# Kernel optimization log

Measured on AMD Instinct MI355X. Metric: run time of the kernel, lower is better.

The kernel has to match this reference:

```python
import jax, jax.numpy as jnp
import numpy as np

N = 50000
IN_DIM, HID_DIM, OUT_DIM = 16, 64, 32


def setup_inputs() -> dict:
    key = jax.random.key(0)
    k1, k2, k3, k4, k5 = jax.random.split(key, 5)
    x = jax.random.normal(k1, (N, IN_DIM), dtype=jnp.float32)
    edge_index = jax.random.randint(k2, (2, 800000), 0, N, dtype=jnp.int64)
    # GCNConv weights (glorot-ish scale) and biases
    W1 = jax.random.normal(k3, (IN_DIM, HID_DIM), dtype=jnp.float32) / np.sqrt(IN_DIM)
    b1 = jnp.zeros((HID_DIM,), dtype=jnp.float32)
    W2 = jax.random.normal(k4, (HID_DIM, OUT_DIM), dtype=jnp.float32) / np.sqrt(HID_DIM)
    b2 = jnpplus = jnp.zeros((OUT_DIM,), dtype=jnp.float32)
    return {"x": x, "edge_index": edge_index, "W1": W1, "b1": b1, "W2": W2, "b2": b2}


def _gcn_conv(x, src, dst, norm, W, b, num_nodes):
    # PyG GCNConv: h = X W; out[d] = sum_e norm_e * h[src_e]; out += b
    h = x @ W                                   # [N, D_out] small GEMM
    msgs = h[src] * norm[:, None]               # [E+N, D_out] gather (memory-bound)
    out = jax.ops.segment_sum(msgs, dst, num_segments=num_nodes)  # scatter-add
    return out + b


def reference(x, edge_index, W1, b1, W2, b2):
    num_nodes = x.shape[0]
    # add self-loops (PyG GCNConv default add_self_loops=True)
    loops = jnp.arange(num_nodes, dtype=edge_index.dtype)
    src = jnp.concatenate([edge_index[0], loops])
    dst = jnp.concatenate([edge_index[1], loops])
    # symmetric normalization D^{-1/2} (A+I) D^{-1/2}, degree over dst
    deg = jax.ops.segment_sum(jnp.ones_like(src, dtype=x.dtype), dst, num_segments=num_nodes)
    dinv = jnp.where(deg > 0, jax.lax.rsqrt(deg), 0.0)
    norm = dinv[src] * dinv[dst]                # [E+N]

    h = _gcn_conv(x, src, dst, norm, W1, b1, num_nodes)
    h = jax.nn.relu(h)
    out = _gcn_conv(h, src, dst, norm, W2, b2, num_nodes)
    return out
```

## Files before the change

kernel.cpp:

```cpp
#include <hip/hip_runtime.h>
#include <hip/hip_fp16.h>

#define IN_DIM  16
#define HID_DIM 64
#define OUT_DIM 32

#define CAP   8192
#define EPB   3328
#define CONVB 64

__device__ __forceinline__ int detect_is64(const void* edges) {
    const int* w = (const int*)edges;
    int is64 = 1;
    #pragma unroll
    for (int i = 0; i < 16; ++i) is64 &= (w[2 * i + 1] == 0);
    return is64;
}

__device__ __forceinline__ long long edge_at(const void* edges, int is64, long long i) {
    if (is64) return ((const long long*)edges)[i];
    return (long long)((const int*)edges)[i];
}

__global__ __launch_bounds__(256) void k_partA(const void* edges, int* gcur,
                                               unsigned int* gpart, int nbuk, long long E,
                                               const float* __restrict__ x,
                                               __half* __restrict__ xh,
                                               long long xElems, int nblkA) {
    if (blockIdx.x >= nblkA) {
        const float4* x4 = (const float4*)x;
        uint2* outp = (uint2*)xh;
        long long n4 = xElems >> 2;
        for (long long i = (long long)(blockIdx.x - nblkA) * 256 + threadIdx.x;
             i < n4; i += (long long)CONVB * 256) {
            float4 v = x4[i];
            __half2 a = __floats2half2_rn(v.x, v.y);
            __half2 b = __floats2half2_rn(v.z, v.w);
            outp[i] = make_uint2(*(unsigned int*)&a, *(unsigned int*)&b);
        }
        return;
    }

    __shared__ unsigned int staged[EPB];
    __shared__ int hcnt[256], hoff[256], hcur[256];
    __shared__ int s64s;
    int t = threadIdx.x;
    if (t == 0) s64s = detect_is64(edges);
    hcnt[t] = 0;
    __syncthreads();
    int is64 = s64s;

    long long e0 = (long long)blockIdx.x * EPB;
    unsigned int rs[13], rd[13];
    int nval = 0;
    #pragma unroll
    for (int k = 0; k < 13; ++k) {
        long long e = e0 + t + k * 256;
        if (e < E) {
            rs[k] = (unsigned int)edge_at(edges, is64, e);
            rd[k] = (unsigned int)edge_at(edges, is64, E + e);
            atomicAdd(&hcnt[rd[k] >> 8], 1);
            nval = k + 1;
        }
    }
    __syncthreads();

    int v = hcnt[t];
    hoff[t] = v;
    __syncthreads();
    for (int d = 1; d < 256; d <<= 1) {
        int u = (t >= d) ? hoff[t - d] : 0;
        __syncthreads();
        hoff[t] += u;
        __syncthreads();
    }
    int excl = hoff[t] - v;
    hoff[t] = excl;
    hcur[t] = excl;
    __syncthreads();

    #pragma unroll
    for (int k = 0; k < 13; ++k) {
        if (k < nval) {
            int p = atomicAdd(&hcur[rd[k] >> 8], 1);
            staged[p] = rs[k] | ((rd[k] & 255u) << 16);
        }
    }
    __syncthreads();

    if (t < nbuk) {
        int c = hcnt[t];
        if (c > 0) {
            int base = atomicAdd(&gcur[t], c);
            int o = hoff[t];
            for (int k = 0; k < c; ++k) {
                int idx = base + k;
                if (idx < CAP) gpart[(size_t)t * CAP + idx] = staged[o + k];
            }
        }
    }
}

__global__ __launch_bounds__(256) void k_partB(const int* __restrict__ gcur,
                                               const unsigned int* __restrict__ gpart,
                                               unsigned short* __restrict__ csr,
                                               int* __restrict__ offs,
                                               float* __restrict__ dinv,
                                               int nbuk, int N) {
    __shared__ unsigned int ebuf[CAP];
    __shared__ int bscan[256];
    __shared__ int hcnt[256], hoff[256], hcur[256];
    int t = threadIdx.x;
    int b = blockIdx.x;

    int bc = (t < nbuk) ? min(gcur[t], CAP) : 0;
    bscan[t] = bc;
    hcnt[t] = 0;
    __syncthreads();
    for (int d = 1; d < 256; d <<= 1) {
        int u = (t >= d) ? bscan[t - d] : 0;
        __syncthreads();
        bscan[t] += u;
        __syncthreads();
    }
    int base = (b == 0) ? 0 : bscan[b - 1];
    int cnt  = bscan[b] - base;

    for (int i = t; i < cnt; i += 256) ebuf[i] = gpart[(size_t)b * CAP + i];
    __syncthreads();
    for (int i = t; i < cnt; i += 256) atomicAdd(&hcnt[(ebuf[i] >> 16) & 255u], 1);
    __syncthreads();

    int v = hcnt[t];
    hoff[t] = v;
    __syncthreads();
    for (int d = 1; d < 256; d <<= 1) {
        int u = (t >= d) ? hoff[t - d] : 0;
        __syncthreads();
        hoff[t] += u;
        __syncthreads();
    }
    int excl = hoff[t] - v;
    hcur[t] = excl;
    __syncthreads();

    int node = b * 256 + t;
    if (node < N) {
        offs[node] = base + excl;
        dinv[node] = rsqrtf((float)v + 1.0f);
    }
    if (b == nbuk - 1 && t == 0) offs[N] = bscan[nbuk - 1];

    for (int i = t; i < cnt; i += 256) {
        unsigned int e = ebuf[i];
        int dl = (e >> 16) & 255;
        int p = atomicAdd(&hcur[dl], 1);
        csr[base + p] = (unsigned short)(e & 0xffffu);
    }
}

#define ASTR 17
#define H1S  68
__global__ __launch_bounds__(256) void k_agg1g(
    const __half* __restrict__ xh, const float* __restrict__ dinv,
    const int* __restrict__ offs, const unsigned short* __restrict__ csr,
    const float* __restrict__ W1, const float* __restrict__ b1,
    const float* __restrict__ W2, __half* __restrict__ h2, int N)
{
    __shared__ __align__(16) float W1s[IN_DIM * HID_DIM];
    __shared__ __align__(16) float W2s[HID_DIM * OUT_DIM];
    __shared__ float b1s[HID_DIM];
    __shared__ __align__(16) float aggs[16 * ASTR];
    __shared__ __align__(16) float h1s[16 * H1S];

    int tid = threadIdx.x;
    for (int i = tid; i < IN_DIM * HID_DIM; i += 256) W1s[i] = W1[i];
    for (int i = tid; i < HID_DIM * OUT_DIM; i += 256) W2s[i] = W2[i];
    if (tid < HID_DIM) b1s[tid] = b1[tid];

    int lane = tid & 63;
    int g = lane >> 4, sub = lane & 15;
    int comp = sub >> 3;
    int way  = sub & 7;
    int nl   = (tid >> 6) * 4 + g;
    int node = blockIdx.x * 16 + nl;

    float acc[8] = {0.f, 0.f, 0.f, 0.f, 0.f, 0.f, 0.f, 0.f};
    float di = 0.f;
    if (node < N) {
        const uint4* x2 = (const uint4*)xh;
        di = dinv[node];
        int start = offs[node], end = offs[node + 1];
        if (way == 0) {
            uint4 r = x2[(size_t)node * 2 + comp];
            const __half2* hp = (const __half2*)&r;
            #pragma unroll
            for (int c = 0; c < 4; ++c) {
                float2 f = __half22float2(hp[c]);
                acc[c * 2]     = di * f.x;
                acc[c * 2 + 1] = di * f.y;
            }
        }
        int j = start + way;
        for (; j + 8 < end; j += 16) {
            int s0 = csr[j], s1 = csr[j + 8];
            float w0 = dinv[s0], w1 = dinv[s1];
            uint4 r0 = x2[(size_t)s0 * 2 + comp];
            uint4 r1 = x2[(size_t)s1 * 2 + comp];
            const __half2* hp0 = (const __half2*)&r0;
            const __half2* hp1 = (const __half2*)&r1;
            #pragma unroll
            for (int c = 0; c < 4; ++c) {
                float2 f0 = __half22float2(hp0[c]);
                float2 f1 = __half22float2(hp1[c]);
                acc[c * 2]     += w0 * f0.x + w1 * f1.x;
                acc[c * 2 + 1] += w0 * f0.y + w1 * f1.y;
            }
        }
        if (j < end) {
            int s = csr[j];
            float w = dinv[s];
            uint4 r = x2[(size_t)s * 2 + comp];
            const __half2* hp = (const __half2*)&r;
            #pragma unroll
            for (int c = 0; c < 4; ++c) {
                float2 f = __half22float2(hp[c]);
                acc[c * 2]     += w * f.x;
                acc[c * 2 + 1] += w * f.y;
            }
        }
        #pragma unroll
        for (int m = 1; m <= 4; m <<= 1) {
            #pragma unroll
            for (int c = 0; c < 8; ++c) acc[c] += __shfl_xor(acc[c], m, 64);
        }
    }
    if (way == 0) {
        #pragma unroll
        for (int c = 0; c < 8; ++c) aggs[nl * ASTR + comp * 8 + c] = di * acc[c];
    }
    __syncthreads();

    int nl2 = tid >> 4, q = tid & 15;

    float a1[4];
    #pragma unroll
    for (int c = 0; c < 4; ++c) a1[c] = b1s[q * 4 + c];
    #pragma unroll
    for (int k = 0; k < IN_DIM; ++k) {
        float a = aggs[nl2 * ASTR + k];
        float4 w = *(const float4*)&W1s[k * HID_DIM + q * 4];
        a1[0] += a * w.x; a1[1] += a * w.y; a1[2] += a * w.z; a1[3] += a * w.w;
    }
    *(float4*)&h1s[nl2 * H1S + q * 4] =
        make_float4(fmaxf(a1[0], 0.f), fmaxf(a1[1], 0.f),
                    fmaxf(a1[2], 0.f), fmaxf(a1[3], 0.f));
    __syncthreads();

    float a2x = 0.f, a2y = 0.f;
    const float4* h1row = (const float4*)&h1s[nl2 * H1S];
    #pragma unroll
    for (int k4 = 0; k4 < 16; ++k4) {
        float4 hv = h1row[k4];
        const float* wb = &W2s[(k4 * 4) * OUT_DIM + q * 2];
        float2 w0 = *(const float2*)(wb);
        float2 w1 = *(const float2*)(wb + OUT_DIM);
        float2 w2 = *(const float2*)(wb + 2 * OUT_DIM);
        float2 w3 = *(const float2*)(wb + 3 * OUT_DIM);
        a2x += hv.x * w0.x + hv.y * w1.x + hv.z * w2.x + hv.w * w3.x;
        a2y += hv.x * w0.y + hv.y * w1.y + hv.z * w2.y + hv.w * w3.y;
    }
    int gn = blockIdx.x * 16 + nl2;
    if (gn < N) {
        __half2 p = __floats2half2_rn(a2x, a2y);
        ((unsigned int*)h2)[(size_t)gn * 16 + q] = *(unsigned int*)&p;
    }
}

__global__ __launch_bounds__(256) void k_agg2(
    const __half* __restrict__ h2, const float* __restrict__ dinv,
    const int* __restrict__ offs, const unsigned short* __restrict__ csr,
    const float* __restrict__ b2, float* __restrict__ out, int N)
{
    int gtid = blockIdx.x * 256 + threadIdx.x;
    int lane = gtid & 63;
    int g = lane >> 4, sub = lane & 15;
    int comp = sub & 3, way = sub >> 2;
    int node = (gtid >> 6) * 4 + g;
    if (node >= N) return;
    const uint4* h24 = (const uint4*)h2;
    float di = dinv[node];
    int start = offs[node], end = offs[node + 1];
    float acc[8] = {0.f, 0.f, 0.f, 0.f, 0.f, 0.f, 0.f, 0.f};
    if (way == 0) {
        uint4 r = h24[(size_t)node * 4 + comp];
        const __half2* hp = (const __half2*)&r;
        #pragma unroll
        for (int c = 0; c < 4; ++c) {
            float2 f = __half22float2(hp[c]);
            acc[c * 2]     = di * f.x;
            acc[c * 2 + 1] = di * f.y;
        }
    }
    int j = start + way;
    for (; j + 4 < end; j += 8) {
        int s0 = csr[j], s1 = csr[j + 4];
        float w0 = dinv[s0], w1 = dinv[s1];
        uint4 r0 = h24[(size_t)s0 * 4 + comp];
        uint4 r1 = h24[(size_t)s1 * 4 + comp];
        const __half2* hp0 = (const __half2*)&r0;
        const __half2* hp1 = (const __half2*)&r1;
        #pragma unroll
        for (int c = 0; c < 4; ++c) {
            float2 f0 = __half22float2(hp0[c]);
            float2 f1 = __half22float2(hp1[c]);
            acc[c * 2]     += w0 * f0.x + w1 * f1.x;
            acc[c * 2 + 1] += w0 * f0.y + w1 * f1.y;
        }
    }
    if (j < end) {
        int s = csr[j];
        float w = dinv[s];
        uint4 r = h24[(size_t)s * 4 + comp];
        const __half2* hp = (const __half2*)&r;
        #pragma unroll
        for (int c = 0; c < 4; ++c) {
            float2 f = __half22float2(hp[c]);
            acc[c * 2]     += w * f.x;
            acc[c * 2 + 1] += w * f.y;
        }
    }
    #pragma unroll
    for (int m = 4; m <= 8; m <<= 1) {
        #pragma unroll
        for (int c = 0; c < 8; ++c) acc[c] += __shfl_xor(acc[c], m, 64);
    }
    if (way == 0) {
        const float4* b24 = (const float4*)b2;
        float4 bb0 = b24[comp * 2], bb1 = b24[comp * 2 + 1];
        float4* out4 = (float4*)out;
        out4[(size_t)node * 8 + comp * 2 + 0] =
            make_float4(di * acc[0] + bb0.x, di * acc[1] + bb0.y,
                        di * acc[2] + bb0.z, di * acc[3] + bb0.w);
        out4[(size_t)node * 8 + comp * 2 + 1] =
            make_float4(di * acc[4] + bb1.x, di * acc[5] + bb1.y,
                        di * acc[6] + bb1.z, di * acc[7] + bb1.w);
    }
}

extern "C" void kernel_launch(void* const* d_in, const int* in_sizes, int n_in,
                              void* d_out, int out_size, void* d_ws, size_t ws_size,
                              hipStream_t stream) {
    const float* x     = (const float*)d_in[0];
    const void*  edges = d_in[1];
    const float* W1    = (const float*)d_in[2];
    const float* b1    = (const float*)d_in[3];
    const float* W2    = (const float*)d_in[4];
    const float* b2    = (const float*)d_in[5];
    float* out = (float*)d_out;

    const int       N = in_sizes[0] / IN_DIM;
    const long long E = in_sizes[1] / 2;
    const int    NBUK = (N + 255) >> 8;
    const int   NBLKA = (int)((E + EPB - 1) / EPB);

    unsigned short* csr   = (unsigned short*)d_ws;
    unsigned int*   gpart = (unsigned int*)(csr + ((E + 7) & ~7LL));
    __half* xh       = (__half*)(gpart + (size_t)NBUK * CAP);
    __half* h2       = (__half*)(xh + (size_t)IN_DIM * N);
    float*  dinv     = (float*)(h2 + (size_t)OUT_DIM * N);
    int*    offs     = (int*)(dinv + N);
    int*    gcur     = offs + N + 1;

    const int B = 256;
    hipMemsetAsync(gcur, 0, (size_t)NBUK * sizeof(int), stream);
    k_partA<<<NBLKA + CONVB, B, 0, stream>>>(edges, gcur, gpart, NBUK, E,
                                             x, xh, (long long)N * IN_DIM, NBLKA);
    k_partB<<<NBUK, B, 0, stream>>>(gcur, gpart, csr, offs, dinv, NBUK, N);

    k_agg1g<<<(N + 15) / 16, B, 0, stream>>>(xh, dinv, offs, csr,
                                             W1, b1, W2, h2, N);
    k_agg2<<<(N + 15) / 16, B, 0, stream>>>(h2, dinv, offs, csr, b2, out, N);
}
```

Baseline: 137.2 us.

## Use wavefront shuffle scans, hoist CSR loads, add occupancy launch bounds

Replaces the shared-memory Hillis-Steele scans (sixteen block barriers each) in the partition kernels with a wave-level shuffle scan followed by a short cross-wave combine. It also moves the dinv/offs loads in k_agg1g ahead of the weight staging so their latency overlaps it. It adds min-blocks-per-CU hints to the two aggregation kernels to raise occupancy. The hints may force register spills.

```diff
diff --git a/kernel.cpp b/kernel.cpp
--- a/kernel.cpp
+++ b/kernel.cpp
@@ -20,6 +20,23 @@
 __device__ __forceinline__ long long edge_at(const void* edges, int is64, long long i) {
     if (is64) return ((const long long*)edges)[i];
     return (long long)((const int*)edges)[i];
+}
+
+__device__ __forceinline__ int block_incl_scan(int v, int t, int* wsum) {
+    int lane = t & 63, w = t >> 6;
+    int s = v;
+    #pragma unroll
+    for (int d = 1; d < 64; d <<= 1) {
+        int u = __shfl_up(s, d, 64);
+        if (lane >= d) s += u;
+    }
+    if (lane == 63) wsum[w] = s;
+    __syncthreads();
+    int add = 0;
+    #pragma unroll
+    for (int i = 0; i < 4; ++i)
+        if (i < w) add += wsum[i];
+    return s + add;
 }
 
 __global__ __launch_bounds__(256) void k_partA(const void* edges, int* gcur,
@@ -43,6 +60,7 @@
 
     __shared__ unsigned int staged[EPB];
     __shared__ int hcnt[256], hoff[256], hcur[256];
+    __shared__ int wsum[4];
     __shared__ int s64s;
     int t = threadIdx.x;
     if (t == 0) s64s = detect_is64(edges);
@@ -66,15 +84,8 @@
     __syncthreads();
 
     int v = hcnt[t];
-    hoff[t] = v;
-    __syncthreads();
-    for (int d = 1; d < 256; d <<= 1) {
-        int u = (t >= d) ? hoff[t - d] : 0;
-        __syncthreads();
-        hoff[t] += u;
-        __syncthreads();
-    }
-    int excl = hoff[t] - v;
+    int incl = block_incl_scan(v, t, wsum);
+    int excl = incl - v;
     hoff[t] = excl;
     hcur[t] = excl;
     __syncthreads();
@@ -109,20 +120,16 @@
                                                int nbuk, int N) {
     __shared__ unsigned int ebuf[CAP];
     __shared__ int bscan[256];
-    __shared__ int hcnt[256], hoff[256], hcur[256];
+    __shared__ int hcnt[256], hcur[256];
+    __shared__ int wsum[4];
     int t = threadIdx.x;
     int b = blockIdx.x;
 
     int bc = (t < nbuk) ? min(gcur[t], CAP) : 0;
-    bscan[t] = bc;
     hcnt[t] = 0;
-    __syncthreads();
-    for (int d = 1; d < 256; d <<= 1) {
-        int u = (t >= d) ? bscan[t - d] : 0;
-        __syncthreads();
-        bscan[t] += u;
-        __syncthreads();
-    }
+    int bincl = block_incl_scan(bc, t, wsum);
+    bscan[t] = bincl;
+    __syncthreads();
     int base = (b == 0) ? 0 : bscan[b - 1];
     int cnt  = bscan[b] - base;
 
@@ -132,15 +139,8 @@
     __syncthreads();
 
     int v = hcnt[t];
-    hoff[t] = v;
-    __syncthreads();
-    for (int d = 1; d < 256; d <<= 1) {
-        int u = (t >= d) ? hoff[t - d] : 0;
-        __syncthreads();
-        hoff[t] += u;
-        __syncthreads();
-    }
-    int excl = hoff[t] - v;
+    int incl = block_incl_scan(v, t, wsum);
+    int excl = incl - v;
     hcur[t] = excl;
     __syncthreads();
 
@@ -161,7 +161,7 @@
 
 #define ASTR 17
 #define H1S  68
-__global__ __launch_bounds__(256) void k_agg1g(
+__global__ __launch_bounds__(256, 6) void k_agg1g(
     const __half* __restrict__ xh, const float* __restrict__ dinv,
     const int* __restrict__ offs, const unsigned short* __restrict__ csr,
     const float* __restrict__ W1, const float* __restrict__ b1,
@@ -174,10 +174,6 @@
     __shared__ __align__(16) float h1s[16 * H1S];
 
     int tid = threadIdx.x;
-    for (int i = tid; i < IN_DIM * HID_DIM; i += 256) W1s[i] = W1[i];
-    for (int i = tid; i < HID_DIM * OUT_DIM; i += 256) W2s[i] = W2[i];
-    if (tid < HID_DIM) b1s[tid] = b1[tid];
-
     int lane = tid & 63;
     int g = lane >> 4, sub = lane & 15;
     int comp = sub >> 3;
@@ -185,12 +181,21 @@
     int nl   = (tid >> 6) * 4 + g;
     int node = blockIdx.x * 16 + nl;
 
+    float di = 0.f;
+    int start = 0, end = 0;
+    if (node < N) {
+        di = dinv[node];
+        start = offs[node];
+        end = offs[node + 1];
+    }
+
+    for (int i = tid; i < IN_DIM * HID_DIM; i += 256) W1s[i] = W1[i];
+    for (int i = tid; i < HID_DIM * OUT_DIM; i += 256) W2s[i] = W2[i];
+    if (tid < HID_DIM) b1s[tid] = b1[tid];
+
     float acc[8] = {0.f, 0.f, 0.f, 0.f, 0.f, 0.f, 0.f, 0.f};
-    float di = 0.f;
     if (node < N) {
         const uint4* x2 = (const uint4*)xh;
-        di = dinv[node];
-        int start = offs[node], end = offs[node + 1];
         if (way == 0) {
             uint4 r = x2[(size_t)node * 2 + comp];
             const __half2* hp = (const __half2*)&r;
@@ -277,7 +282,7 @@
     }
 }
 
-__global__ __launch_bounds__(256) void k_agg2(
+__global__ __launch_bounds__(256, 8) void k_agg2(
     const __half* __restrict__ h2, const float* __restrict__ dinv,
     const int* __restrict__ offs, const unsigned short* __restrict__ csr,
     const float* __restrict__ b2, float* __restrict__ out, int N)
```

New measurement: 133.9 us. -2.4%, faster.
